# Optimization experiments

Measured on AMD Instinct MI355X. Metric: run time of the kernel, lower is better.

The kernel has to match this reference:

```python
import jax, jax.numpy as jnp
import numpy as np

STALK_DIM = 16
N_NODES = 50000
N_EDGES = 400000
HIDDEN = 64


def setup_inputs() -> dict:
    key = jax.random.key(0)
    k1, k2, k3, k4 = jax.random.split(key, 4)
    d = STALK_DIM
    x = jax.random.normal(k1, (N_NODES, d), dtype=jnp.float32)
    edge_index = jax.random.randint(k2, (2, N_EDGES), 0, N_NODES, dtype=jnp.int64)
    W1 = jax.random.normal(k3, (HIDDEN, 2 * d), dtype=jnp.float32) * (1.0 / np.sqrt(2 * d))
    b1 = jnp.zeros((HIDDEN,), dtype=jnp.float32)
    W2 = jax.random.normal(k4, (d, HIDDEN), dtype=jnp.float32) * (1.0 / np.sqrt(HIDDEN))
    b2 = jnp.zeros((d,), dtype=jnp.float32)
    return {"x": x, "edge_index": edge_index, "W1": W1, "b1": b1, "W2": W2, "b2": b2}


def reference(x, edge_index, W1, b1, W2, b2):
    d = x.shape[1]
    n = x.shape[0]
    src, dst = edge_index[0], edge_index[1]
    xs, xd = x[src], x[dst]  # [E, d]

    def reflection(a, b):
        h = jax.nn.relu(jnp.concatenate([a, b], axis=1) @ W1.T + b1)
        return h @ W2.T + b2  # [E, d]

    def householder(v):
        # F.normalize(v, dim=1): v / max(||v||, 1e-12)
        vn = v / jnp.maximum(jnp.linalg.norm(v, axis=1, keepdims=True), 1e-12)
        return jnp.eye(d, dtype=v.dtype)[None] - 2.0 * vn[:, :, None] * vn[:, None, :]

    F_s = householder(reflection(xs, xd))  # [E, d, d]
    F_d = householder(reflection(xd, xs))  # [E, d, d]
    L_sd = -jnp.einsum('eki,ekj->eij', F_s, F_d)  # -F_s^T @ F_d, [E, d, d]

    # degrees: both endpoints of every edge contribute 1
    ones_e = jnp.ones(src.shape[0], dtype=x.dtype)
    deg = jnp.zeros(n, dtype=x.dtype).at[src].add(ones_e).at[dst].add(ones_e)
    deg_inv_sqrt = 1.0 / jnp.sqrt(jnp.maximum(deg, 1e-5))
    # D_inv_sqrt is scalar*I per node, so normalization is a scalar coefficient per edge
    coef = deg_inv_sqrt[src] * deg_inv_sqrt[dst]  # [E]

    # out[s] -= D^-1/2_s L D^-1/2_d x[d] ; out[d] -= D^-1/2_d L^T D^-1/2_s x[s]
    msg_s = coef[:, None] * jnp.einsum('eij,ej->ei', L_sd, xd)  # goes to src
    msg_d = coef[:, None] * jnp.einsum('eji,ej->ei', L_sd, xs)  # goes to dst

    out = x - jnp.zeros_like(x).at[src].add(msg_s) - jnp.zeros_like(x).at[dst].add(msg_d)
    return jax.nn.relu(out)
```

## Files before the change

### kernel.cpp

```cpp
#include <hip/hip_runtime.h>
#include <hip/hip_bf16.h>

#define N_NODES 50000
#define N_EDGES 400000
#define D 16
#define HID 64

#define SCAN_B 256
#define SCAN_G ((N_NODES + SCAN_B - 1) / SCAN_B)

typedef unsigned short ushort_t;

#define CNT4_OFF  0
#define DEG_OFF   (4 * N_NODES)
#define OFF_OFF   (5 * N_NODES)
#define CUR_OFF   (6 * N_NODES + 1)
#define BS_OFF    (7 * N_NODES + 1)
#define FLAGS_I   (BS_OFF + SCAN_G)
#define MSG_OFF_I (((FLAGS_I + 2) + 3) & ~3)
#define CSR_NEEDED_BYTES ((size_t)(MSG_OFF_I + 2 * N_EDGES * D) * 4 + 64)

#define FB_NDEG   (N_NODES)
#define FB_NACC   (N_NODES * D)
#define FB_FLAGS  (FB_NDEG + FB_NACC)

__device__ __forceinline__ float bf_bits(ushort_t us) {
    return __uint_as_float(((unsigned)us) << 16);
}
__device__ __forceinline__ ushort_t f2bf(float v) {
    unsigned u = __float_as_uint(v);
    unsigned r = (u + 0x7fffu + ((u >> 16) & 1u)) >> 16;
    return (ushort_t)r;
}
__device__ __forceinline__ float ld_f(const void* p, int idx, int f32) {
    return f32 ? ((const float*)p)[idx]
               : bf_bits(((const ushort_t*)p)[idx]);
}

__device__ __forceinline__ void load16(const void* __restrict__ p, long long base,
                                       int f32, float* o) {
    if (f32) {
        const float4* q = (const float4*)((const float*)p + base);
        float4 a = q[0], b = q[1], c = q[2], d = q[3];
        o[0]=a.x; o[1]=a.y; o[2]=a.z; o[3]=a.w;
        o[4]=b.x; o[5]=b.y; o[6]=b.z; o[7]=b.w;
        o[8]=c.x; o[9]=c.y; o[10]=c.z; o[11]=c.w;
        o[12]=d.x; o[13]=d.y; o[14]=d.z; o[15]=d.w;
    } else {
        const uint4* q = (const uint4*)((const ushort_t*)p + base);
        uint4 a = q[0], b = q[1];
        unsigned u[8] = {a.x, a.y, a.z, a.w, b.x, b.y, b.z, b.w};
#pragma unroll
        for (int k = 0; k < 8; k++) {
            o[2 * k]     = __uint_as_float(u[k] << 16);
            o[2 * k + 1] = __uint_as_float(u[k] & 0xffff0000u);
        }
    }
}

__device__ __forceinline__ void load_edge(const void* __restrict__ ei, int e, int is64,
                                          int& s, int& d) {
    if (is64) {
        const long long* p = (const long long*)ei;
        s = (int)p[e];
        d = (int)p[N_EDGES + e];
    } else {
        const int* p = (const int*)ei;
        s = p[e];
        d = p[N_EDGES + e];
    }
}

__device__ __forceinline__ void detect_flags(const void* x, const void* ei, int* flags) {
    const ushort_t* h = (const ushort_t*)x;
    int f32 = 0;
    for (int k = 0; k < 256; k++) {
        float v = bf_bits(h[k]);
        if (!(v == v) || fabsf(v) > 1.0e6f) { f32 = 1; break; }
    }
    const long long* p = (const long long*)ei;
    int i64 = 1;
    for (int k = 0; k < 16; k++) {
        long long v = p[k];
        if (v < 0 || v >= N_NODES) { i64 = 0; break; }
    }
    flags[0] = f32;
    flags[1] = i64;
}

__device__ __forceinline__ void stage_weights(
    const void* W1, const void* b1, const void* W2, const void* b2, int f32,
    float* sW1, float* sW2t, float* sb1, float* sb2)
{
    int t = threadIdx.x;
    for (int idx = t; idx < HID * 2 * D; idx += blockDim.x)
        sW1[idx] = ld_f(W1, idx, f32);
    for (int idx = t; idx < HID * D; idx += blockDim.x) {
        int j = idx / D, i = idx % D;
        sW2t[idx] = ld_f(W2, i * HID + j, f32);
    }
    if (t < HID) sb1[t] = ld_f(b1, t, f32);
    if (t < D)  sb2[t] = ld_f(b2, t, f32);
}

__device__ __forceinline__ void edge_math_v4(
    const float* __restrict__ sW1, const float* __restrict__ sW2t,
    const float* __restrict__ sb1, const float* __restrict__ sb2,
    const float* xs, const float* xd, float coef,
    float* ms, float* md)
{
    float vs[D], vd[D];
#pragma unroll
    for (int i = 0; i < D; i++) { vs[i] = sb2[i]; vd[i] = sb2[i]; }

#pragma unroll 4
    for (int j = 0; j < HID; j++) {
        float hs = sb1[j], hd = sb1[j];
        const float4* w4 = (const float4*)&sW1[j * 2 * D];
#pragma unroll
        for (int t = 0; t < 4; t++) {
            float4 wv = w4[t];
            int k = 4 * t;
            hs = fmaf(wv.x, xs[k],     hs); hd = fmaf(wv.x, xd[k],     hd);
            hs = fmaf(wv.y, xs[k + 1], hs); hd = fmaf(wv.y, xd[k + 1], hd);
            hs = fmaf(wv.z, xs[k + 2], hs); hd = fmaf(wv.z, xd[k + 2], hd);
            hs = fmaf(wv.w, xs[k + 3], hs); hd = fmaf(wv.w, xd[k + 3], hd);
        }
#pragma unroll
        for (int t = 0; t < 4; t++) {
            float4 wv = w4[4 + t];
            int k = 4 * t;
            hs = fmaf(wv.x, xd[k],     hs); hd = fmaf(wv.x, xs[k],     hd);
            hs = fmaf(wv.y, xd[k + 1], hs); hd = fmaf(wv.y, xs[k + 1], hd);
            hs = fmaf(wv.z, xd[k + 2], hs); hd = fmaf(wv.z, xs[k + 2], hd);
            hs = fmaf(wv.w, xd[k + 3], hs); hd = fmaf(wv.w, xs[k + 3], hd);
        }
        hs = fmaxf(hs, 0.0f);
        hd = fmaxf(hd, 0.0f);
        const float4* w24 = (const float4*)&sW2t[j * D];
#pragma unroll
        for (int t = 0; t < 4; t++) {
            float4 u = w24[t];
            int i = 4 * t;
            vs[i]     = fmaf(u.x, hs, vs[i]);     vd[i]     = fmaf(u.x, hd, vd[i]);
            vs[i + 1] = fmaf(u.y, hs, vs[i + 1]); vd[i + 1] = fmaf(u.y, hd, vd[i + 1]);
            vs[i + 2] = fmaf(u.z, hs, vs[i + 2]); vd[i + 2] = fmaf(u.z, hd, vd[i + 2]);
            vs[i + 3] = fmaf(u.w, hs, vs[i + 3]); vd[i + 3] = fmaf(u.w, hd, vd[i + 3]);
        }
    }

    float ns = 0.0f, nd = 0.0f;
#pragma unroll
    for (int i = 0; i < D; i++) { ns = fmaf(vs[i], vs[i], ns); nd = fmaf(vd[i], vd[i], nd); }
    float is_ = 1.0f / fmaxf(sqrtf(ns), 1e-12f);
    float id_ = 1.0f / fmaxf(sqrtf(nd), 1e-12f);
#pragma unroll
    for (int i = 0; i < D; i++) { vs[i] *= is_; vd[i] *= id_; }

    float dot1 = 0.0f;
#pragma unroll
    for (int i = 0; i < D; i++) dot1 = fmaf(vd[i], xd[i], dot1);
#pragma unroll
    for (int i = 0; i < D; i++) ms[i] = fmaf(-2.0f * dot1, vd[i], xd[i]);
    float dot2 = 0.0f;
#pragma unroll
    for (int i = 0; i < D; i++) dot2 = fmaf(vs[i], ms[i], dot2);
#pragma unroll
    for (int i = 0; i < D; i++) ms[i] = coef * fmaf(-2.0f * dot2, vs[i], ms[i]);

    float dot3 = 0.0f;
#pragma unroll
    for (int i = 0; i < D; i++) dot3 = fmaf(vs[i], xs[i], dot3);
#pragma unroll
    for (int i = 0; i < D; i++) md[i] = fmaf(-2.0f * dot3, vs[i], xs[i]);
    float dot4 = 0.0f;
#pragma unroll
    for (int i = 0; i < D; i++) dot4 = fmaf(vd[i], md[i], dot4);
#pragma unroll
    for (int i = 0; i < D; i++) md[i] = coef * fmaf(-2.0f * dot4, vd[i], md[i]);
}

__global__ void csr_init_kernel(int* __restrict__ wsI,
                                const void* __restrict__ x,
                                const void* __restrict__ ei) {
    int i = blockIdx.x * blockDim.x + threadIdx.x;
    if (i < 4 * N_NODES) wsI[CNT4_OFF + i] = 0;
    if (blockIdx.x == 0 && threadIdx.x == 0)
        detect_flags(x, ei, wsI + FLAGS_I);
}

__global__ void csr_count_kernel(const void* __restrict__ ei, int* __restrict__ wsI) {
    int i64 = wsI[FLAGS_I + 1];
    int e = blockIdx.x * blockDim.x + threadIdx.x;
    if (e >= N_EDGES) return;
    int s, d;
    load_edge(ei, e, i64, s, d);
    int r = (e & 3) * N_NODES;
    atomicAdd(&wsI[CNT4_OFF + r + s], 1);
    atomicAdd(&wsI[CNT4_OFF + r + d], 1);
}

__global__ __launch_bounds__(SCAN_B) void csr_scan1_kernel(int* __restrict__ wsI) {
    __shared__ int sm[SCAN_B];
    int t = threadIdx.x;
    int g = blockIdx.x * SCAN_B + t;
    int c = 0;
    if (g < N_NODES) {
        c = wsI[CNT4_OFF + g] + wsI[CNT4_OFF + N_NODES + g]
          + wsI[CNT4_OFF + 2 * N_NODES + g] + wsI[CNT4_OFF + 3 * N_NODES + g];
        wsI[DEG_OFF + g] = c;
    }
    sm[t] = c;
    __syncthreads();
    for (int st = SCAN_B / 2; st > 0; st >>= 1) {
        if (t < st) sm[t] += sm[t + st];
        __syncthreads();
    }
    if (t == 0) wsI[BS_OFF + blockIdx.x] = sm[0];
}

__global__ __launch_bounds__(SCAN_B) void csr_scan3_kernel(int* __restrict__ wsI) {
    __shared__ int sB[SCAN_B];
    __shared__ int sm[SCAN_B];
    int t = threadIdx.x;
    int bsv = (t < SCAN_G) ? wsI[BS_OFF + t] : 0;
    sB[t] = bsv;
    __syncthreads();
    for (int st = 1; st < SCAN_B; st <<= 1) {
        int u = (t >= st) ? sB[t - st] : 0;
        __syncthreads();
        sB[t] += u;
        __syncthreads();
    }
    int blockBase = sB[blockIdx.x] - wsI[BS_OFF + blockIdx.x];

    int g = blockIdx.x * SCAN_B + t;
    int c = (g < N_NODES) ? wsI[DEG_OFF + g] : 0;
    sm[t] = c;
    __syncthreads();
    for (int st = 1; st < SCAN_B; st <<= 1) {
        int u = (t >= st) ? sm[t - st] : 0;
        __syncthreads();
        sm[t] += u;
        __syncthreads();
    }
    int excl = sm[t] - c + blockBase;
    if (g < N_NODES) {
        wsI[OFF_OFF + g] = excl;
        wsI[CUR_OFF + g] = excl;
        if (g == N_NODES - 1) wsI[OFF_OFF + N_NODES] = excl + c;
    }
}

__global__ __launch_bounds__(256) void csr_edge_kernel(
    const void* __restrict__ x,
    const void* __restrict__ ei,
    const void* __restrict__ W1,
    const void* __restrict__ b1,
    const void* __restrict__ W2,
    const void* __restrict__ b2,
    int* __restrict__ wsI)
{
    __shared__ __align__(16) float sW1[HID * 2 * D];
    __shared__ __align__(16) float sW2t[HID * D];
    __shared__ float sb1[HID];
    __shared__ float sb2[D];

    int f32 = wsI[FLAGS_I];
    int i64 = wsI[FLAGS_I + 1];
    stage_weights(W1, b1, W2, b2, f32, sW1, sW2t, sb1, sb2);
    __syncthreads();

    int e = blockIdx.x * blockDim.x + threadIdx.x;
    if (e >= N_EDGES) return;

    int s, d;
    load_edge(ei, e, i64, s, d);

    float xs[D], xd[D];
    load16(x, (long long)s * D, f32, xs);
    load16(x, (long long)d * D, f32, xd);

    float degs = (float)wsI[DEG_OFF + s];
    float degd = (float)wsI[DEG_OFF + d];
    float coef = (1.0f / sqrtf(fmaxf(degs, 1e-5f))) * (1.0f / sqrtf(fmaxf(degd, 1e-5f)));

    float ms[D], md[D];
    edge_math_v4(sW1, sW2t, sb1, sb2, xs, xd, coef, ms, md);

    float* msg = (float*)(wsI + MSG_OFF_I);
    int slot_s = atomicAdd(&wsI[CUR_OFF + s], 1);
    float4* m0 = (float4*)(msg + (long long)slot_s * D);
    m0[0] = make_float4(ms[0], ms[1], ms[2], ms[3]);
    m0[1] = make_float4(ms[4], ms[5], ms[6], ms[7]);
    m0[2] = make_float4(ms[8], ms[9], ms[10], ms[11]);
    m0[3] = make_float4(ms[12], ms[13], ms[14], ms[15]);
    int slot_d = atomicAdd(&wsI[CUR_OFF + d], 1);
    float4* m1 = (float4*)(msg + (long long)slot_d * D);
    m1[0] = make_float4(md[0], md[1], md[2], md[3]);
    m1[1] = make_float4(md[4], md[5], md[6], md[7]);
    m1[2] = make_float4(md[8], md[9], md[10], md[11]);
    m1[3] = make_float4(md[12], md[13], md[14], md[15]);
}

__global__ __launch_bounds__(256) void csr_gather_kernel(
    const void* __restrict__ x,
    const int* __restrict__ wsI,
    void* __restrict__ out)
{
    int f32 = wsI[FLAGS_I];
    int n = blockIdx.x * 64 + (threadIdx.x >> 2);
    int c = threadIdx.x & 3;
    if (n >= N_NODES) return;

    const int* off = wsI + OFF_OFF;
    const float4* msg4 = (const float4*)(wsI + MSG_OFF_I);

    int beg = off[n], end = off[n + 1];
    float4 a = make_float4(0.0f, 0.0f, 0.0f, 0.0f);
    int it = beg;
    for (; it + 2 <= end; it += 2) {
        float4 u = msg4[(long long)it * 4 + c];
        float4 v = msg4[(long long)(it + 1) * 4 + c];
        a.x += u.x + v.x; a.y += u.y + v.y; a.z += u.z + v.z; a.w += u.w + v.w;
    }
    if (it < end) {
        float4 u = msg4[(long long)it * 4 + c];
        a.x += u.x; a.y += u.y; a.z += u.z; a.w += u.w;
    }

    long long xb = (long long)n * D + 4 * c;
    float4 xv;
    if (f32) {
        xv = *(const float4*)((const float*)x + xb);
    } else {
        uint2 u = *(const uint2*)((const ushort_t*)x + xb);
        xv.x = __uint_as_float(u.x << 16);
        xv.y = __uint_as_float(u.x & 0xffff0000u);
        xv.z = __uint_as_float(u.y << 16);
        xv.w = __uint_as_float(u.y & 0xffff0000u);
    }
    float4 r;
    r.x = fmaxf(xv.x + a.x, 0.0f);
    r.y = fmaxf(xv.y + a.y, 0.0f);
    r.z = fmaxf(xv.z + a.z, 0.0f);
    r.w = fmaxf(xv.w + a.w, 0.0f);
    if (f32) {
        *(float4*)((float*)out + xb) = r;
    } else {
        uint2 o;
        o.x = (unsigned)f2bf(r.x) | ((unsigned)f2bf(r.y) << 16);
        o.y = (unsigned)f2bf(r.z) | ((unsigned)f2bf(r.w) << 16);
        *(uint2*)((ushort_t*)out + xb) = o;
    }
}

__global__ void fb_init_kernel(float* __restrict__ ws,
                               const void* __restrict__ x,
                               const void* __restrict__ ei) {
    int i = blockIdx.x * blockDim.x + threadIdx.x;
    if (i < FB_FLAGS) ws[i] = 0.0f;
    if (blockIdx.x == 0 && threadIdx.x == 0)
        detect_flags(x, ei, (int*)(ws + FB_FLAGS));
}

__global__ void fb_deg_kernel(const void* __restrict__ ei, float* __restrict__ ws) {
    int i64 = ((const int*)(ws + FB_FLAGS))[1];
    int e = blockIdx.x * blockDim.x + threadIdx.x;
    if (e >= N_EDGES) return;
    int s, d;
    load_edge(ei, e, i64, s, d);
    atomicAdd(&ws[s], 1.0f);
    atomicAdd(&ws[d], 1.0f);
}

__global__ __launch_bounds__(256) void fb_edge_kernel(
    const void* __restrict__ x, const void* __restrict__ ei,
    const void* __restrict__ W1, const void* __restrict__ b1,
    const void* __restrict__ W2, const void* __restrict__ b2,
    float* __restrict__ ws)
{
    __shared__ __align__(16) float sW1[HID * 2 * D];
    __shared__ __align__(16) float sW2t[HID * D];
    __shared__ float sb1[HID];
    __shared__ float sb2[D];
    const int* flags = (const int*)(ws + FB_FLAGS);
    int f32 = flags[0], i64 = flags[1];
    stage_weights(W1, b1, W2, b2, f32, sW1, sW2t, sb1, sb2);
    __syncthreads();
    int e = blockIdx.x * blockDim.x + threadIdx.x;
    if (e >= N_EDGES) return;
    int s, d;
    load_edge(ei, e, i64, s, d);
    float xs[D], xd[D];
    load16(x, (long long)s * D, f32, xs);
    load16(x, (long long)d * D, f32, xd);
    float coef = (1.0f / sqrtf(fmaxf(ws[s], 1e-5f))) * (1.0f / sqrtf(fmaxf(ws[d], 1e-5f)));
    float ms[D], md[D];
    edge_math_v4(sW1, sW2t, sb1, sb2, xs, xd, coef, ms, md);
    float* acc = ws + FB_NDEG;
#pragma unroll
    for (int i = 0; i < D; i++) atomicAdd(&acc[(long long)s * D + i], ms[i]);
#pragma unroll
    for (int i = 0; i < D; i++) atomicAdd(&acc[(long long)d * D + i], md[i]);
}

__global__ void fb_finalize_kernel(const void* __restrict__ x,
                                   const float* __restrict__ ws,
                                   void* __restrict__ out)
{
    int f32 = ((const int*)(ws + FB_FLAGS))[0];
    const float* acc = ws + FB_NDEG;
    int i = blockIdx.x * blockDim.x + threadIdx.x;
    if (i >= FB_NACC) return;
    float v = ld_f(x, i, f32) + acc[i];
    v = fmaxf(v, 0.0f);
    if (f32) ((float*)out)[i] = v;
    else     ((__hip_bfloat16*)out)[i] = __float2bfloat16(v);
}

extern "C" void kernel_launch(void* const* d_in, const int* in_sizes, int n_in,
                              void* d_out, int out_size, void* d_ws, size_t ws_size,
                              hipStream_t stream)
{
    const void* x  = d_in[0];
    const void* ei = d_in[1];
    const void* W1 = d_in[2];
    const void* b1 = d_in[3];
    const void* W2 = d_in[4];
    const void* b2 = d_in[5];

    int blk = 256;
    if (ws_size >= CSR_NEEDED_BYTES) {
        int* wsI = (int*)d_ws;
        csr_init_kernel<<<(4 * N_NODES + blk - 1) / blk, blk, 0, stream>>>(wsI, x, ei);
        csr_count_kernel<<<(N_EDGES + blk - 1) / blk, blk, 0, stream>>>(ei, wsI);
        csr_scan1_kernel<<<SCAN_G, SCAN_B, 0, stream>>>(wsI);
        csr_scan3_kernel<<<SCAN_G, SCAN_B, 0, stream>>>(wsI);
        csr_edge_kernel<<<(N_EDGES + blk - 1) / blk, blk, 0, stream>>>(x, ei, W1, b1, W2, b2, wsI);
        csr_gather_kernel<<<(N_NODES + 63) / 64, blk, 0, stream>>>(x, wsI, d_out);
    } else {
        float* ws = (float*)d_ws;
        fb_init_kernel<<<(FB_FLAGS + blk - 1) / blk, blk, 0, stream>>>(ws, x, ei);
        fb_deg_kernel<<<(N_EDGES + blk - 1) / blk, blk, 0, stream>>>(ei, ws);
        fb_edge_kernel<<<(N_EDGES + blk - 1) / blk, blk, 0, stream>>>(x, ei, W1, b1, W2, b2, ws);
        fb_finalize_kernel<<<(FB_NACC + blk - 1) / blk, blk, 0, stream>>>(x, ws, d_out);
    }
}
```

Measured before the change: 201.4 us.

## Use packed fp16 dot2 for edge MLP on bf16 inputs and drop init kernel

Adds a bf16-input path that packs the weights and node features into fp16 pairs and computes the edge MLP with fdot2 instructions, roughly halving the FMA count. The separate init kernel is replaced by a memset, and each kernel re-detects the dtype flags into shared memory instead of reading them from the workspace. For f32 inputs the old scalar path is kept, but shared-memory usage grows because both weight layouts are declared. The fp16 path also reduces precision in the hidden layer.

```diff
diff --git a/kernel.cpp b/kernel.cpp
--- a/kernel.cpp
+++ b/kernel.cpp
@@ -1,5 +1,6 @@
 #include <hip/hip_runtime.h>
 #include <hip/hip_bf16.h>
+#include <hip/hip_fp16.h>
 
 #define N_NODES 50000
 #define N_EDGES 400000
@@ -10,14 +11,14 @@
 #define SCAN_G ((N_NODES + SCAN_B - 1) / SCAN_B)
 
 typedef unsigned short ushort_t;
+typedef _Float16 h16x2 __attribute__((ext_vector_type(2)));
 
 #define CNT4_OFF  0
 #define DEG_OFF   (4 * N_NODES)
 #define OFF_OFF   (5 * N_NODES)
 #define CUR_OFF   (6 * N_NODES + 1)
 #define BS_OFF    (7 * N_NODES + 1)
-#define FLAGS_I   (BS_OFF + SCAN_G)
-#define MSG_OFF_I (((FLAGS_I + 2) + 3) & ~3)
+#define MSG_OFF_I (((BS_OFF + SCAN_G) + 3) & ~3)
 #define CSR_NEEDED_BYTES ((size_t)(MSG_OFF_I + 2 * N_EDGES * D) * 4 + 64)
 
 #define FB_NDEG   (N_NODES)
@@ -27,6 +28,8 @@
 __device__ __forceinline__ float bf_bits(ushort_t us) {
     return __uint_as_float(((unsigned)us) << 16);
 }
+__device__ __forceinline__ float lo_bf(unsigned u) { return __uint_as_float(u << 16); }
+__device__ __forceinline__ float hi_bf(unsigned u) { return __uint_as_float(u & 0xffff0000u); }
 __device__ __forceinline__ ushort_t f2bf(float v) {
     unsigned u = __float_as_uint(v);
     unsigned r = (u + 0x7fffu + ((u >> 16) & 1u)) >> 16;
@@ -35,6 +38,39 @@
 __device__ __forceinline__ float ld_f(const void* p, int idx, int f32) {
     return f32 ? ((const float*)p)[idx]
                : bf_bits(((const ushort_t*)p)[idx]);
+}
+
+__device__ __forceinline__ unsigned pack_h2(float a, float b) {
+#if __has_builtin(__builtin_amdgcn_cvt_pkrtz)
+    return __builtin_bit_cast(unsigned, __builtin_amdgcn_cvt_pkrtz(a, b));
+#else
+    h16x2 h;
+    h.x = (_Float16)a;
+    h.y = (_Float16)b;
+    return __builtin_bit_cast(unsigned, h);
+#endif
+}
+
+#if __has_builtin(__builtin_amdgcn_fdot2)
+__device__ __forceinline__ float fdot2u(unsigned a, unsigned b, float c) {
+    return __builtin_amdgcn_fdot2(__builtin_bit_cast(h16x2, a),
+                                  __builtin_bit_cast(h16x2, b), c, false);
+}
+#else
+__device__ __forceinline__ float fdot2u(unsigned a, unsigned b, float c) {
+    h16x2 ha = __builtin_bit_cast(h16x2, a);
+    h16x2 hb = __builtin_bit_cast(h16x2, b);
+    return fmaf((float)ha.x, (float)hb.x, fmaf((float)ha.y, (float)hb.y, c));
+}
+#endif
+
+__device__ __forceinline__ void ld16u(const unsigned* __restrict__ p, unsigned* o) {
+    const uint4* q = (const uint4*)p;
+    uint4 a = q[0], b = q[1], c = q[2], d = q[3];
+    o[0]=a.x; o[1]=a.y; o[2]=a.z; o[3]=a.w;
+    o[4]=b.x; o[5]=b.y; o[6]=b.z; o[7]=b.w;
+    o[8]=c.x; o[9]=c.y; o[10]=c.z; o[11]=c.w;
+    o[12]=d.x; o[13]=d.y; o[14]=d.z; o[15]=d.w;
 }
 
 __device__ __forceinline__ void load16(const void* __restrict__ p, long long base,
@@ -52,8 +88,8 @@
         unsigned u[8] = {a.x, a.y, a.z, a.w, b.x, b.y, b.z, b.w};
 #pragma unroll
         for (int k = 0; k < 8; k++) {
-            o[2 * k]     = __uint_as_float(u[k] << 16);
-            o[2 * k + 1] = __uint_as_float(u[k] & 0xffff0000u);
+            o[2 * k]     = lo_bf(u[k]);
+            o[2 * k + 1] = hi_bf(u[k]);
         }
     }
 }
@@ -112,7 +148,6 @@
     float vs[D], vd[D];
 #pragma unroll
     for (int i = 0; i < D; i++) { vs[i] = sb2[i]; vd[i] = sb2[i]; }
-
 #pragma unroll 4
     for (int j = 0; j < HID; j++) {
         float hs = sb1[j], hd = sb1[j];
@@ -148,7 +183,6 @@
             vs[i + 3] = fmaf(u.w, hs, vs[i + 3]); vd[i + 3] = fmaf(u.w, hd, vd[i + 3]);
         }
     }
-
     float ns = 0.0f, nd = 0.0f;
 #pragma unroll
     for (int i = 0; i < D; i++) { ns = fmaf(vs[i], vs[i], ns); nd = fmaf(vd[i], vd[i], nd); }
@@ -156,7 +190,6 @@
     float id_ = 1.0f / fmaxf(sqrtf(nd), 1e-12f);
 #pragma unroll
     for (int i = 0; i < D; i++) { vs[i] *= is_; vd[i] *= id_; }
-
     float dot1 = 0.0f;
 #pragma unroll
     for (int i = 0; i < D; i++) dot1 = fmaf(vd[i], xd[i], dot1);
@@ -167,7 +200,6 @@
     for (int i = 0; i < D; i++) dot2 = fmaf(vs[i], ms[i], dot2);
 #pragma unroll
     for (int i = 0; i < D; i++) ms[i] = coef * fmaf(-2.0f * dot2, vs[i], ms[i]);
-
     float dot3 = 0.0f;
 #pragma unroll
     for (int i = 0; i < D; i++) dot3 = fmaf(vs[i], xs[i], dot3);
@@ -180,17 +212,13 @@
     for (int i = 0; i < D; i++) md[i] = coef * fmaf(-2.0f * dot4, vd[i], md[i]);
 }
 
-__global__ void csr_init_kernel(int* __restrict__ wsI,
-                                const void* __restrict__ x,
-                                const void* __restrict__ ei) {
-    int i = blockIdx.x * blockDim.x + threadIdx.x;
-    if (i < 4 * N_NODES) wsI[CNT4_OFF + i] = 0;
-    if (blockIdx.x == 0 && threadIdx.x == 0)
-        detect_flags(x, ei, wsI + FLAGS_I);
-}
-
-__global__ void csr_count_kernel(const void* __restrict__ ei, int* __restrict__ wsI) {
-    int i64 = wsI[FLAGS_I + 1];
+__global__ void csr_count_kernel(const void* __restrict__ ei,
+                                 const void* __restrict__ x,
+                                 int* __restrict__ wsI) {
+    __shared__ int sfl[2];
+    if (threadIdx.x == 0) detect_flags(x, ei, sfl);
+    __syncthreads();
+    int i64 = sfl[1];
     int e = blockIdx.x * blockDim.x + threadIdx.x;
     if (e >= N_EDGES) return;
     int s, d;
@@ -261,54 +289,193 @@
     const void* __restrict__ b2,
     int* __restrict__ wsI)
 {
-    __shared__ __align__(16) float sW1[HID * 2 * D];
-    __shared__ __align__(16) float sW2t[HID * D];
+    __shared__ __align__(16) unsigned sW1h[HID * 16];
+    __shared__ __align__(16) unsigned sW2h[32 * 16];
     __shared__ float sb1[HID];
     __shared__ float sb2[D];
-
-    int f32 = wsI[FLAGS_I];
-    int i64 = wsI[FLAGS_I + 1];
-    stage_weights(W1, b1, W2, b2, f32, sW1, sW2t, sb1, sb2);
-    __syncthreads();
-
-    int e = blockIdx.x * blockDim.x + threadIdx.x;
+    __shared__ __align__(16) float sW1f[HID * 2 * D];
+    __shared__ __align__(16) float sW2tf[HID * D];
+    __shared__ int sfl[2];
+
+    if (threadIdx.x == 0) detect_flags(x, ei, sfl);
+    __syncthreads();
+    int f32 = sfl[0], i64 = sfl[1];
+    int t = threadIdx.x;
+
+    if (!f32) {
+        const ushort_t* W1b = (const ushort_t*)W1;
+        for (int idx = t; idx < HID * 16; idx += 256) {
+            int j = idx >> 4, tt = idx & 15;
+            sW1h[idx] = pack_h2(bf_bits(W1b[j * 32 + 2 * tt]),
+                                bf_bits(W1b[j * 32 + 2 * tt + 1]));
+        }
+        const ushort_t* W2b = (const ushort_t*)W2;
+        for (int idx = t; idx < 32 * 16; idx += 256) {
+            int jj = idx >> 4, i = idx & 15;
+            sW2h[idx] = pack_h2(bf_bits(W2b[i * HID + 2 * jj]),
+                                bf_bits(W2b[i * HID + 2 * jj + 1]));
+        }
+    } else {
+        for (int idx = t; idx < HID * 2 * D; idx += 256)
+            sW1f[idx] = ld_f(W1, idx, 1);
+        for (int idx = t; idx < HID * D; idx += 256) {
+            int j = idx / D, i = idx % D;
+            sW2tf[idx] = ld_f(W2, i * HID + j, 1);
+        }
+    }
+    if (t < HID) sb1[t] = ld_f(b1, t, f32);
+    if (t < D)  sb2[t] = ld_f(b2, t, f32);
+    __syncthreads();
+
+    int e = blockIdx.x * 256 + t;
     if (e >= N_EDGES) return;
 
     int s, d;
     load_edge(ei, e, i64, s, d);
-
-    float xs[D], xd[D];
-    load16(x, (long long)s * D, f32, xs);
-    load16(x, (long long)d * D, f32, xd);
-
     float degs = (float)wsI[DEG_OFF + s];
     float degd = (float)wsI[DEG_OFF + d];
     float coef = (1.0f / sqrtf(fmaxf(degs, 1e-5f))) * (1.0f / sqrtf(fmaxf(degd, 1e-5f)));
-
-    float ms[D], md[D];
-    edge_math_v4(sW1, sW2t, sb1, sb2, xs, xd, coef, ms, md);
-
     float* msg = (float*)(wsI + MSG_OFF_I);
-    int slot_s = atomicAdd(&wsI[CUR_OFF + s], 1);
-    float4* m0 = (float4*)(msg + (long long)slot_s * D);
-    m0[0] = make_float4(ms[0], ms[1], ms[2], ms[3]);
-    m0[1] = make_float4(ms[4], ms[5], ms[6], ms[7]);
-    m0[2] = make_float4(ms[8], ms[9], ms[10], ms[11]);
-    m0[3] = make_float4(ms[12], ms[13], ms[14], ms[15]);
-    int slot_d = atomicAdd(&wsI[CUR_OFF + d], 1);
-    float4* m1 = (float4*)(msg + (long long)slot_d * D);
-    m1[0] = make_float4(md[0], md[1], md[2], md[3]);
-    m1[1] = make_float4(md[4], md[5], md[6], md[7]);
-    m1[2] = make_float4(md[8], md[9], md[10], md[11]);
-    m1[3] = make_float4(md[12], md[13], md[14], md[15]);
+
+    if (!f32) {
+        unsigned xsh[8], xdh[8];
+        {
+            const uint4* q = (const uint4*)((const ushort_t*)x + (long long)s * D);
+            uint4 a = q[0], b = q[1];
+            unsigned u[8] = {a.x, a.y, a.z, a.w, b.x, b.y, b.z, b.w};
+#pragma unroll
+            for (int k = 0; k < 8; k++) xsh[k] = pack_h2(lo_bf(u[k]), hi_bf(u[k]));
+        }
+        {
+            const uint4* q = (const uint4*)((const ushort_t*)x + (long long)d * D);
+            uint4 a = q[0], b = q[1];
+            unsigned u[8] = {a.x, a.y, a.z, a.w, b.x, b.y, b.z, b.w};
+#pragma unroll
+            for (int k = 0; k < 8; k++) xdh[k] = pack_h2(lo_bf(u[k]), hi_bf(u[k]));
+        }
+
+        float vs[D], vd[D];
+#pragma unroll
+        for (int i = 0; i < D; i++) { vs[i] = sb2[i]; vd[i] = sb2[i]; }
+
+#pragma unroll 2
+        for (int jj = 0; jj < 32; jj++) {
+            unsigned wr[32];
+            ld16u(&sW1h[(2 * jj) * 16], wr);
+            ld16u(&sW1h[(2 * jj) * 16 + 16], wr + 16);
+            unsigned w2r[16];
+            ld16u(&sW2h[jj * 16], w2r);
+
+            float hs0 = sb1[2 * jj],     hd0 = hs0;
+            float hs1 = sb1[2 * jj + 1], hd1 = hs1;
+#pragma unroll
+            for (int k = 0; k < 8; k++) {
+                hs0 = fdot2u(wr[k],      xsh[k], hs0);
+                hd0 = fdot2u(wr[k],      xdh[k], hd0);
+                hs1 = fdot2u(wr[16 + k], xsh[k], hs1);
+                hd1 = fdot2u(wr[16 + k], xdh[k], hd1);
+            }
+#pragma unroll
+            for (int k = 0; k < 8; k++) {
+                hs0 = fdot2u(wr[8 + k],  xdh[k], hs0);
+                hd0 = fdot2u(wr[8 + k],  xsh[k], hd0);
+                hs1 = fdot2u(wr[24 + k], xdh[k], hs1);
+                hd1 = fdot2u(wr[24 + k], xsh[k], hd1);
+            }
+            hs0 = fmaxf(hs0, 0.0f); hd0 = fmaxf(hd0, 0.0f);
+            hs1 = fmaxf(hs1, 0.0f); hd1 = fmaxf(hd1, 0.0f);
+            unsigned hsp = pack_h2(hs0, hs1);
+            unsigned hdp = pack_h2(hd0, hd1);
+#pragma unroll
+            for (int i = 0; i < D; i++) {
+                vs[i] = fdot2u(w2r[i], hsp, vs[i]);
+                vd[i] = fdot2u(w2r[i], hdp, vd[i]);
+            }
+        }
+
+        float xs[D], xd[D];
+#pragma unroll
+        for (int k = 0; k < 8; k++) {
+            h16x2 a = __builtin_bit_cast(h16x2, xsh[k]);
+            xs[2 * k] = (float)a.x; xs[2 * k + 1] = (float)a.y;
+            h16x2 b = __builtin_bit_cast(h16x2, xdh[k]);
+            xd[2 * k] = (float)b.x; xd[2 * k + 1] = (float)b.y;
+        }
+
+        float ns = 0.0f, nd = 0.0f;
+#pragma unroll
+        for (int i = 0; i < D; i++) { ns = fmaf(vs[i], vs[i], ns); nd = fmaf(vd[i], vd[i], nd); }
+        float is_ = 1.0f / fmaxf(sqrtf(ns), 1e-12f);
+        float id_ = 1.0f / fmaxf(sqrtf(nd), 1e-12f);
+#pragma unroll
+        for (int i = 0; i < D; i++) { vs[i] *= is_; vd[i] *= id_; }
+
+        float ms[D], md[D];
+        float dot1 = 0.0f;
+#pragma unroll
+        for (int i = 0; i < D; i++) dot1 = fmaf(vd[i], xd[i], dot1);
+#pragma unroll
+        for (int i = 0; i < D; i++) ms[i] = fmaf(-2.0f * dot1, vd[i], xd[i]);
+        float dot2 = 0.0f;
+#pragma unroll
+        for (int i = 0; i < D; i++) dot2 = fmaf(vs[i], ms[i], dot2);
+#pragma unroll
+        for (int i = 0; i < D; i++) ms[i] = coef * fmaf(-2.0f * dot2, vs[i], ms[i]);
+        float dot3 = 0.0f;
+#pragma unroll
+        for (int i = 0; i < D; i++) dot3 = fmaf(vs[i], xs[i], dot3);
+#pragma unroll
+        for (int i = 0; i < D; i++) md[i] = fmaf(-2.0f * dot3, vs[i], xs[i]);
+        float dot4 = 0.0f;
+#pragma unroll
+        for (int i = 0; i < D; i++) dot4 = fmaf(vd[i], md[i], dot4);
+#pragma unroll
+        for (int i = 0; i < D; i++) md[i] = coef * fmaf(-2.0f * dot4, vd[i], md[i]);
+
+        int slot_s = atomicAdd(&wsI[CUR_OFF + s], 1);
+        float4* m0 = (float4*)(msg + (long long)slot_s * D);
+        m0[0] = make_float4(ms[0], ms[1], ms[2], ms[3]);
+        m0[1] = make_float4(ms[4], ms[5], ms[6], ms[7]);
+        m0[2] = make_float4(ms[8], ms[9], ms[10], ms[11]);
+        m0[3] = make_float4(ms[12], ms[13], ms[14], ms[15]);
+        int slot_d = atomicAdd(&wsI[CUR_OFF + d], 1);
+        float4* m1 = (float4*)(msg + (long long)slot_d * D);
+        m1[0] = make_float4(md[0], md[1], md[2], md[3]);
+        m1[1] = make_float4(md[4], md[5], md[6], md[7]);
+        m1[2] = make_float4(md[8], md[9], md[10], md[11]);
+        m1[3] = make_float4(md[12], md[13], md[14], md[15]);
+    } else {
+        float xs[D], xd[D];
+        load16(x, (long long)s * D, 1, xs);
+        load16(x, (long long)d * D, 1, xd);
+        float ms[D], md[D];
+        edge_math_v4(sW1f, sW2tf, sb1, sb2, xs, xd, coef, ms, md);
+        int slot_s = atomicAdd(&wsI[CUR_OFF + s], 1);
+        float4* m0 = (float4*)(msg + (long long)slot_s * D);
+        m0[0] = make_float4(ms[0], ms[1], ms[2], ms[3]);
+        m0[1] = make_float4(ms[4], ms[5], ms[6], ms[7]);
+        m0[2] = make_float4(ms[8], ms[9], ms[10], ms[11]);
+        m0[3] = make_float4(ms[12], ms[13], ms[14], ms[15]);
+        int slot_d = atomicAdd(&wsI[CUR_OFF + d], 1);
+        float4* m1 = (float4*)(msg + (long long)slot_d * D);
+        m1[0] = make_float4(md[0], md[1], md[2], md[3]);
+        m1[1] = make_float4(md[4], md[5], md[6], md[7]);
+        m1[2] = make_float4(md[8], md[9], md[10], md[11]);
+        m1[3] = make_float4(md[12], md[13], md[14], md[15]);
+    }
 }
 
 __global__ __launch_bounds__(256) void csr_gather_kernel(
     const void* __restrict__ x,
+    const void* __restrict__ ei,
     const int* __restrict__ wsI,
     void* __restrict__ out)
 {
-    int f32 = wsI[FLAGS_I];
+    __shared__ int sfl[2];
+    if (threadIdx.x == 0) detect_flags(x, ei, sfl);
+    __syncthreads();
+    int f32 = sfl[0];
+
     int n = blockIdx.x * 64 + (threadIdx.x >> 2);
     int c = threadIdx.x & 3;
     if (n >= N_NODES) return;
@@ -335,10 +502,8 @@
         xv = *(const float4*)((const float*)x + xb);
     } else {
         uint2 u = *(const uint2*)((const ushort_t*)x + xb);
-        xv.x = __uint_as_float(u.x << 16);
-        xv.y = __uint_as_float(u.x & 0xffff0000u);
-        xv.z = __uint_as_float(u.y << 16);
-        xv.w = __uint_as_float(u.y & 0xffff0000u);
+        xv.x = lo_bf(u.x); xv.y = hi_bf(u.x);
+        xv.z = lo_bf(u.y); xv.w = hi_bf(u.y);
     }
     float4 r;
     r.x = fmaxf(xv.x + a.x, 0.0f);
@@ -433,12 +598,12 @@
     int blk = 256;
     if (ws_size >= CSR_NEEDED_BYTES) {
         int* wsI = (int*)d_ws;
-        csr_init_kernel<<<(4 * N_NODES + blk - 1) / blk, blk, 0, stream>>>(wsI, x, ei);
-        csr_count_kernel<<<(N_EDGES + blk - 1) / blk, blk, 0, stream>>>(ei, wsI);
+        hipMemsetAsync(d_ws, 0, (size_t)4 * N_NODES * sizeof(int), stream);
+        csr_count_kernel<<<(N_EDGES + blk - 1) / blk, blk, 0, stream>>>(ei, x, wsI);
         csr_scan1_kernel<<<SCAN_G, SCAN_B, 0, stream>>>(wsI);
         csr_scan3_kernel<<<SCAN_G, SCAN_B, 0, stream>>>(wsI);
         csr_edge_kernel<<<(N_EDGES + blk - 1) / blk, blk, 0, stream>>>(x, ei, W1, b1, W2, b2, wsI);
-        csr_gather_kernel<<<(N_NODES + 63) / 64, blk, 0, stream>>>(x, wsI, d_out);
+        csr_gather_kernel<<<(N_NODES + 63) / 64, blk, 0, stream>>>(x, ei, wsI, d_out);
     } else {
         float* ws = (float*)d_ws;
         fb_init_kernel<<<(FB_FLAGS + blk - 1) / blk, blk, 0, stream>>>(ws, x, ei);
```

Result: no change. 200.7 us, median of 3 (-0.3%).
